# Kernel tuning notes

Measured on AMD Instinct MI355X. Metric: run time of the kernel, lower is better.

## Reference

```python
import jax, jax.numpy as jnp
import numpy as np
from jax import lax

E = 8          # num_experts
K = 2          # top-k
TASKS = 8
GATE_DIM = 16
# (in, expand, out, kernel, stride) per MoE stage
STAGES = [(3, 32, 16, 7, 2), (16, 64, 32, 3, 1), (32, 128, 64, 3, 2), (64, 256, 64, 3, 1), (64, 128, 32, 3, 1)]
DN = ('NCHW', 'OIHW', 'NCHW')


def _pw(x, w):
    return lax.conv_general_dilated(x, w, (1, 1), 'VALID', dimension_numbers=DN)


def _dw(x, w, s):
    p = w.shape[-1] // 2
    return lax.conv_general_dilated(x, w, (s, s), [(p, p), (p, p)], dimension_numbers=DN, feature_group_count=x.shape[1])


def _gn(x, scale, bias):
    # GroupNorm with num_groups = C // 4, eps = 1e-5 (torch default)
    B, C, H, W = x.shape
    G = C // 4
    xr = x.reshape(B, G, -1)
    m = xr.mean(-1, keepdims=True)
    v = xr.var(-1, keepdims=True)
    xn = ((xr - m) * lax.rsqrt(v + 1e-5)).reshape(B, C, H, W)
    return xn * scale[None, :, None, None] + bias[None, :, None, None]


def _dsc(x, p, stride):
    # DSCBlock: pw-conv -> GN -> SiLU -> dw-conv -> GN -> SiLU -> pw-conv -> GN
    w1, s1, b1, w2, s2, b2, w3, s3, b3 = p
    x = jax.nn.silu(_gn(_pw(x, w1), s1, b1))
    x = jax.nn.silu(_gn(_dw(x, w2, stride), s2, b2))
    return _gn(_pw(x, w3), s3, b3)


def _moe(gate_input, x, wg, p, stride, task_bh):
    # task-conditioned top-k softmax gating (noisy_gating=False, all aux loss weights 0)
    logits = gate_input @ wg[task_bh]                      # (B, E)
    probs = jax.nn.softmax(logits, axis=-1)
    topv, topi = lax.top_k(probs, K)
    topv = topv / topv.sum(-1, keepdims=True)              # renormalize top-k gates
    Bn = gate_input.shape[0]
    dense = jnp.zeros_like(probs).at[jnp.arange(Bn)[:, None], topi].set(topv)
    eo = jax.vmap(lambda pe: _dsc(x, pe, stride))(p)       # (E, B, C, H, W)
    return jnp.einsum('be,ebchw->bchw', dense, eo)


def _forward(fl, task_bh):
    gi, xi, ppe = fl[0], fl[1], fl[2]
    x = xi
    for i, (_, _, _, _, s) in enumerate(STAGES):
        base = 3 + i * 10
        wg = fl[base]
        p = tuple(fl[base + 1: base + 10])
        x = _moe(gi, x, wg, p, s, task_bh)
    Bn = x.shape[0]
    # patchify: (B,32,20,20) -> unfold(2,4,4).unfold(3,4,4) -> permute -> (B,25,512)
    patches = x.reshape(Bn, 32, 5, 4, 5, 4).transpose(0, 1, 2, 4, 3, 5)  # (B,32,5,5,4,4)
    patches = patches.transpose(0, 2, 3, 4, 5, 1).reshape(Bn, 25, 512)
    return patches + ppe


def setup_inputs():
    key = jax.random.key(0)
    ks = iter(jax.random.split(key, 256))
    B = 64
    d = {}
    d['gate_input'] = jax.random.normal(next(ks), (B, GATE_DIM), jnp.float32)
    d['expert_input'] = jax.random.normal(next(ks), (B, 3, 80, 80), jnp.float32)
    d['patch_pos_embed'] = 0.02 * jax.random.normal(next(ks), (1, 25, 512), jnp.float32)
    for i, (cin, exp, cout, k, s) in enumerate(STAGES, 1):
        d[f's{i}_wg'] = 0.1 * jax.random.normal(next(ks), (TASKS, GATE_DIM, E), jnp.float32)
        d[f's{i}_w1'] = jax.random.normal(next(ks), (E, exp, cin, 1, 1), jnp.float32) / np.sqrt(cin)
        d[f's{i}_g1s'] = 1.0 + 0.1 * jax.random.normal(next(ks), (E, exp), jnp.float32)
        d[f's{i}_g1b'] = 0.1 * jax.random.normal(next(ks), (E, exp), jnp.float32)
        d[f's{i}_w2'] = jax.random.normal(next(ks), (E, exp, 1, k, k), jnp.float32) / k
        d[f's{i}_g2s'] = 1.0 + 0.1 * jax.random.normal(next(ks), (E, exp), jnp.float32)
        d[f's{i}_g2b'] = 0.1 * jax.random.normal(next(ks), (E, exp), jnp.float32)
        d[f's{i}_w3'] = jax.random.normal(next(ks), (E, cout, exp, 1, 1), jnp.float32) / np.sqrt(exp)
        d[f's{i}_g3s'] = 1.0 + 0.1 * jax.random.normal(next(ks), (E, cout), jnp.float32)
        d[f's{i}_g3b'] = 0.1 * jax.random.normal(next(ks), (E, cout), jnp.float32)
    d['task_bh'] = 3
    return d


def reference(gate_input, expert_input, patch_pos_embed, s1_wg, s1_w1, s1_g1s, s1_g1b, s1_w2, s1_g2s, s1_g2b, s1_w3, s1_g3s, s1_g3b, s2_wg, s2_w1, s2_g1s, s2_g1b, s2_w2, s2_g2s, s2_g2b, s2_w3, s2_g3s, s2_g3b, s3_wg, s3_w1, s3_g1s, s3_g1b, s3_w2, s3_g2s, s3_g2b, s3_w3, s3_g3s, s3_g3b, s4_wg, s4_w1, s4_g1s, s4_g1b, s4_w2, s4_g2s, s4_g2b, s4_w3, s4_g3s, s4_g3b, s5_wg, s5_w1, s5_g1s, s5_g1b, s5_w2, s5_g2s, s5_g2b, s5_w3, s5_g3s, s5_g3b, task_bh):
    fl = (gate_input, expert_input, patch_pos_embed,
          s1_wg, s1_w1, s1_g1s, s1_g1b, s1_w2, s1_g2s, s1_g2b, s1_w3, s1_g3s, s1_g3b,
          s2_wg, s2_w1, s2_g1s, s2_g1b, s2_w2, s2_g2s, s2_g2b, s2_w3, s2_g3s, s2_g3b,
          s3_wg, s3_w1, s3_g1s, s3_g1b, s3_w2, s3_g2s, s3_g2b, s3_w3, s3_g3s, s3_g3b,
          s4_wg, s4_w1, s4_g1s, s4_g1b, s4_w2, s4_g2s, s4_g2b, s4_w3, s4_g3s, s4_g3b,
          s5_wg, s5_w1, s5_g1s, s5_g1b, s5_w2, s5_g2s, s5_g2b, s5_w3, s5_g3s, s5_g3b)
    patches = _forward(fl, task_bh)
    loss = jnp.zeros((), patches.dtype)  # all MoE loss weights are 0 in VisionEncoder
    return (patches, loss)
```

## Files before the change

### kernel.cpp

```cpp
#include <hip/hip_runtime.h>
#include <cstddef>

#define TPB 256

typedef __attribute__((ext_vector_type(8))) short short8v;
typedef __attribute__((ext_vector_type(4))) float f32x4;

__device__ __forceinline__ int rfl(int v) { return __builtin_amdgcn_readfirstlane(v); }
__device__ __forceinline__ float rflf(float v) {
    return __int_as_float(__builtin_amdgcn_readfirstlane(__float_as_int(v)));
}

__device__ __forceinline__ unsigned short f2bf(float f) {
    union { float f; unsigned int u; } x{f};
    unsigned int r = x.u + 0x7fffu + ((x.u >> 16) & 1u);
    return (unsigned short)(r >> 16);
}
__device__ __forceinline__ float bf2f(unsigned short u) {
    return __uint_as_float(((unsigned int)u) << 16);
}

template <int N, int NW>
__device__ __forceinline__ void bredN(float* v, float* red) {
    __syncthreads();
// ... 32 lines not shown
                                             unsigned short* __restrict__ whi) {
    const int sizes[9] = {4096, 8192, 16384, 32768, 65536, 131072, 131072, 65536, 32768};
    int idx = blockIdx.x * 256 + threadIdx.x;
    if (idx >= 487424) return;
    int rem = idx, s = 0;
    while (s < 8 && rem >= sizes[s]) { rem -= sizes[s]; s++; }
    whi[idx] = f2bf(wsrc.p[s][rem]);
}

__global__ void gate_kernel(const float* __restrict__ gi, GatePtrs gp,
                            const int* __restrict__ taskp,
                            int* __restrict__ gidx, float* __restrict__ gw) {
    const int s = blockIdx.x;
    const int b = threadIdx.x;
    const int task = taskp[0];
    const float* wg = gp.wg[s] + (size_t)task * 16 * 8;
    float l[8];
    #pragma unroll
    for (int e = 0; e < 8; e++) l[e] = 0.f;
    for (int d = 0; d < 16; d++) {
        float v = gi[b * 16 + d];
        #pragma unroll
        for (int e = 0; e < 8; e++) l[e] += v * wg[d * 8 + e];
    }
    float mx = l[0];
    #pragma unroll
    for (int e = 1; e < 8; e++) mx = fmaxf(mx, l[e]);
    float p[8]; float sum = 0.f;
    #pragma unroll
    for (int e = 0; e < 8; e++) { p[e] = expf(l[e] - mx); sum += p[e]; }
    int i0 = 0;
    #pragma unroll
    for (int e = 1; e < 8; e++) if (p[e] > p[i0]) i0 = e;
    int i1 = (i0 == 0) ? 1 : 0;
    #pragma unroll
    for (int e = 0; e < 8; e++) if (e != i0 && p[e] > p[i1]) i1 = e;
    const float denom = p[i0] + p[i1];
    const int base = (s * 64 + b) * 2;
    gidx[base] = i0; gidx[base + 1] = i1;
    gw[base] = p[i0] / denom; gw[base + 1] = p[i1] / denom;
}

template <int M, int K, int N, int MT, int NCHK, bool FOLD, bool BIN>
__global__ __launch_bounds__(256) void gemm_bf16(
    const unsigned short* __restrict__ inp,
    const unsigned short* __restrict__ whi,
    const int* __restrict__ gidx, const float* __restrict__ foldStats,
    const float* __restrict__ foldS, const float* __restrict__ foldB,
    unsigned short* __restrict__ outp, float* __restrict__ stats,
    int mfull, int moff, int nchk1) {
    constexpr int KITERS = (K + 31) / 32;
    constexpr int IM = (MT == 64) ? 2 : 1;
    constexpr int IN = (MT == 16) ? 1 : 2;
    const int bx = blockIdx.x;
    const int nc = bx % NCHK, mc = bx / NCHK;
    const int b = blockIdx.y, slot = blockIdx.z;
    const int bs = b * 2 + slot;
    const int e = rfl(gidx[b * 2 + slot]);
    const int n0 = nc * 64, m0 = mc * MT;
    const int tid = threadIdx.x;
    const int lane = tid & 63, wv = tid >> 6;
    const int quad = lane >> 4, l15 = lane & 15;

    __shared__ __align__(16) unsigned short wtile[MT * 40];
    __shared__ unsigned int intile[16 * 65];
    __shared__ float sred[(MT / 4) * 2];
    __shared__ float afv[K], bfv[K];

    if (tid < (MT / 4) * 2) sred[tid] = 0.f;
    if constexpr (FOLD) {
        for (int c = tid; c < K; c += 256) {
            const int g = c >> 2;
            float s1 = 0.f, s2 = 0.f;
            for (int i = 0; i < nchk1; i++) {
                s1 += foldStats[(((size_t)bs * (K / 4) + g) * nchk1 + i) * 2 + 0];
                s2 += foldStats[(((size_t)bs * (K / 4) + g) * nchk1 + i) * 2 + 1];
            }
            const float mean = s1 / (4.f * N);
            const float var = s2 / (4.f * N) - mean * mean;
            const float inv = rsqrtf(var + 1e-5f);
            const float sc = foldS[e * K + c], bi = foldB[e * K + c];
            afv[c] = inv * sc;
            bfv[c] = bi - mean * inv * sc;
        }
    }

    int mbase, nbase;
    if constexpr (MT == 64) { mbase = (wv & 1) * 32; nbase = (wv >> 1) * 32; }
    else if constexpr (MT == 32) { mbase = (wv & 1) * 16; nbase = (wv >> 1) * 32; }
    else { mbase = 0; nbase = wv * 16; }

    f32x4 acc[IM][IN];
    #pragma unroll
    for (int im = 0; im < IM; im++)
        #pragma unroll
        for (int in = 0; in < IN; in++)
            #pragma unroll
            for (int r = 0; r < 4; r++) acc[im][in][r] = 0.f;

    const unsigned short* ib = inp + (size_t)(BIN ? b : bs) * K * N;
    const unsigned short* wbH = whi + ((size_t)e * mfull + moff) * K;

    for (int k0 = 0; k0 < KITERS * 32; k0 += 32) {
        __syncthreads();
        for (int i = tid; i < MT * 32; i += 256) {
            const int m = i >> 5, kk = i & 31;
            const bool ok = (k0 + kk < K);
            wtile[m * 40 + kk] = ok ? wbH[(size_t)(m0 + m) * K + k0 + kk]
                                    : (unsigned short)0;
// ... 45 lines not shown
                    afr[im], bu.s, acc[im][in], 0, 0, 0);
        }
    }

    unsigned short* ob = outp + (size_t)bs * M * N;
    #pragma unroll
    for (int im = 0; im < IM; im++) {
        #pragma unroll
        for (int in = 0; in < IN; in++) {
            const int n = n0 + nbase + in * 16 + l15;
            float s1 = 0.f, s2 = 0.f;
            #pragma unroll
            for (int r = 0; r < 4; r++) {
                const float a = acc[im][in][r];
                s1 += a; s2 += a * a;
            }
            if (n < N) {
                #pragma unroll
                for (int r = 0; r < 4; r++) {
                    const int m = m0 + mbase + im * 16 + quad * 4 + r;
                    ob[(size_t)m * N + n] = f2bf(acc[im][in][r]);
                }
            }
            #pragma unroll
            for (int off = 8; off > 0; off >>= 1) {
                s1 += __shfl_down(s1, off, 16);
                s2 += __shfl_down(s2, off, 16);
            }
            if (l15 == 0) {
                const int gl = (mbase + im * 16) / 4 + quad;
                atomicAdd(&sred[gl * 2 + 0], s1);
                atomicAdd(&sred[gl * 2 + 1], s2);
            }
        }
    }
    __syncthreads();
    for (int i = tid; i < MT / 4; i += 256) {
        float* sp = stats + (((size_t)bs * (mfull / 4) + moff / 4 + mc * (MT / 4) + i)
                             * NCHK + nc) * 2;
        sp[0] = sred[i * 2]; sp[1] = sred[i * 2 + 1];
    }
}

template <int CLOC, int CFULL, int H, int W, int NCH, int TPBk, int NCHK1>
__global__ __launch_bounds__(TPBk) void dw_k(
    const unsigned short* __restrict__ raw1, const float* __restrict__ stats1,
    const float* __restrict__ g1s, const float* __restrict__ g1b,
    const float* __restrict__ w2, const int* __restrict__ gidx,
    unsigned short* __restrict__ act2raw, float* __restrict__ stats2, int coff) {
    constexpr int HW = H * W, HP = H + 2, WPL = W + 3;
    constexpr int NPV = HW / 4, NG = NCH / 4, NW = TPBk / 64;
    constexpr int Qc = HW / 4, QT = NCH * Qc, QI = (QT + TPBk - 1) / TPBk;
    constexpr int G1 = CFULL / 4;
    const int gch = blockIdx.x, b = blockIdx.y, slot = blockIdx.z;
    const int bs = b * 2 + slot;
    const int tid = threadIdx.x;
    const int e = rfl(gidx[b * 2 + slot]);
    const int cb0 = gch * NCH;
    const int cg0 = coff + cb0;

    __shared__ float buf1[NCH * HP * WPL];
    __shared__ float w2s[NCH * 9];
    __shared__ float afl[NCH], bfl[NCH];
    __shared__ float red[2 * NG * NW];

    for (int i = tid; i < NCH * HP * WPL; i += TPBk) buf1[i] = 0.f;
    if (tid < NCH * 9) w2s[tid] = w2[((size_t)e * CFULL + cg0) * 9 + tid];
    if (tid < NCH) {
        const int g = (cg0 + tid) >> 2;
        float s1 = 0.f, s2 = 0.f;
        for (int i = 0; i < NCHK1; i++) {
            s1 += stats1[(((size_t)bs * G1 + g) * NCHK1 + i) * 2 + 0];
            s2 += stats1[(((size_t)bs * G1 + g) * NCHK1 + i) * 2 + 1];
        }
        const float mean = s1 / (4.f * HW);
        const float var = s2 / (4.f * HW) - mean * mean;
        const float inv = rsqrtf(var + 1e-5f);
        const float sc = g1s[e * CFULL + cg0 + tid], bi = g1b[e * CFULL + cg0 + tid];
        afl[tid] = inv * sc; bfl[tid] = bi - mean * inv * sc;
    }
    __syncthreads();

    const unsigned short* rb = raw1 + (size_t)bs * CLOC * HW + (size_t)cb0 * HW;
    for (int i = tid; i < NCH * NPV; i += TPBk) {
        const int c = i / NPV, pv = i - c * NPV;
        const int p4 = pv * 4, ph = p4 / W, pwb = p4 - ph * W;
        const ushort4 u = *(const ushort4*)(rb + (size_t)c * HW + p4);
        const float a = afl[c], bb = bfl[c];
        float* bp = &buf1[(c * HP + ph + 1) * WPL + pwb + 1];
        bp[0] = silu_f(a * bf2f(u.x) + bb);
        bp[1] = silu_f(a * bf2f(u.y) + bb);
        bp[2] = silu_f(a * bf2f(u.z) + bb);
        bp[3] = silu_f(a * bf2f(u.w) + bb);
    }
    __syncthreads();

    float st2[2 * NG];
    #pragma unroll
    for (int i = 0; i < 2 * NG; i++) st2[i] = 0.f;
    unsigned short* ao = act2raw + (size_t)bs * CFULL * HW + (size_t)cg0 * HW;
    #pragma unroll
    for (int qi = 0; qi < QI; qi++) {
        const int q = tid + qi * TPBk;
        if (QI * TPBk == QT || q < QT) {
            const int c = q / Qc, qq = q - c * Qc;
            const int oh = qq % H, owb = (qq / H) * 4;
            float o[4] = {0.f, 0.f, 0.f, 0.f};
            #pragma unroll
            for (int kh = 0; kh < 3; kh++) {
                const int base = (c * HP + oh + kh) * WPL + owb;
                float r[6];
                #pragma unroll
                for (int i = 0; i < 6; i++) r[i] = buf1[base + i];
                const float wa = w2s[c * 9 + kh * 3 + 0];
                const float wb = w2s[c * 9 + kh * 3 + 1];
                const float wcc = w2s[c * 9 + kh * 3 + 2];
                #pragma unroll
                for (int t = 0; t < 4; t++)
                    o[t] += wa * r[t] + wb * r[t + 1] + wcc * r[t + 2];
            }
            ushort4 ov = {f2bf(o[0]), f2bf(o[1]), f2bf(o[2]), f2bf(o[3])};
            *(ushort4*)(ao + c * HW + oh * W + owb) = ov;
            #pragma unroll
            for (int t = 0; t < 4; t++) {
                if constexpr (NG == 1) { st2[0] += o[t]; st2[1] += o[t] * o[t]; }
                else {
                    const bool gs = (c >= 4);
                    float a0 = gs ? 0.f : o[t], a1 = gs ? o[t] : 0.f;
                    st2[0] += a0; st2[1] += a0 * a0;
                    st2[2] += a1; st2[3] += a1 * a1;
                }
            }
        }
    }
    bredN<2 * NG, NW>(st2, red);
    if (tid == 0) {
        #pragma unroll
        for (int g = 0; g < NG; g++) {
            stats2[((size_t)bs * G1 + cg0 / 4 + g) * 2 + 0] = st2[g * 2];
            stats2[((size_t)bs * G1 + cg0 / 4 + g) * 2 + 1] = st2[g * 2 + 1];
        }
    }
}

__global__ __launch_bounds__(256) void s1_stats(
    const float* __restrict__ xin, const float* __restrict__ w1,
    const int* __restrict__ gidx, float* __restrict__ stats1) {
    const int g = blockIdx.x, b = blockIdx.y, slot = blockIdx.z;
    const int tid = threadIdx.x;
    const int e = rfl(gidx[b * 2 + slot]);
    __shared__ float red[8];
    const float* xb = xin + (size_t)b * 3 * 6400;
    const float* w1e = w1 + ((size_t)e * 32 + g * 4) * 3;
    float wr[4][3];
    #pragma unroll
    for (int c = 0; c < 4; c++)
        #pragma unroll
        for (int k = 0; k < 3; k++) wr[c][k] = rflf(w1e[c * 3 + k]);
    float s[2] = {0.f, 0.f};
    #pragma unroll
    for (int j = 0; j < 7; j++) {
        const int i = j * 256 + tid;
        if (i < 1600) {
            const int p4 = i * 4;
            const float4 v0 = *(const float4*)(xb + p4);
            const float4 v1 = *(const float4*)(xb + 6400 + p4);
            const float4 v2 = *(const float4*)(xb + 12800 + p4);
            const float a0[4] = {v0.x, v0.y, v0.z, v0.w};
            const float a1[4] = {v1.x, v1.y, v1.z, v1.w};
            const float a2[4] = {v2.x, v2.y, v2.z, v2.w};
            #pragma unroll
            for (int t = 0; t < 4; t++)
                #pragma unroll
                for (int c = 0; c < 4; c++) {
                    float a = fmaf(wr[c][0], a0[t], fmaf(wr[c][1], a1[t], wr[c][2] * a2[t]));
                    s[0] += a; s[1] += a * a;
                }
        }
    }
    bredN<2, 4>(s, red);
    if (tid == 0) {
        float* sp = stats1 + ((size_t)(b * 2 + slot) * 8 + g) * 2;
        sp[0] = s[0]; sp[1] = s[1];
    }
}

__global__ __launch_bounds__(256) void s1_band(
    const float* __restrict__ xin, const float* __restrict__ w1,
    const float* __restrict__ g1s, const float* __restrict__ g1b,
    const float* __restrict__ w2, const int* __restrict__ gidx,
    const float* __restrict__ stats1,
    unsigned short* __restrict__ rawdw, float* __restrict__ stats2) {
    constexpr int NR = 25, RW = 91, EVO = 44;
    const int gb = blockIdx.x;
    const int g = gb >> 2, band = gb & 3;
    const int b = blockIdx.y, slot = blockIdx.z;
    const int tid = threadIdx.x;
    const int e = rfl(gidx[b * 2 + slot]);

    __shared__ float sbuf[4 * NR * RW];
    __shared__ float w2s[196];
    __shared__ float red[8];

    for (int i = tid; i < 4 * NR * RW; i += 256) sbuf[i] = 0.f;
    if (tid < 196) w2s[tid] = w2[((size_t)e * 32 + g * 4) * 49 + tid];

    const float* sp = stats1 + ((size_t)(b * 2 + slot) * 8 + g) * 2;
    const float s1v = rflf(sp[0]), s2v = rflf(sp[1]);
    const float mean = s1v / 25600.f;
    const float var = s2v / 25600.f - mean * mean;
    const float inv = rsqrtf(var + 1e-5f);

    const float* xb = xin + (size_t)b * 3 * 6400;
    const float* w1e = w1 + ((size_t)e * 32 + g * 4) * 3;
    float wr[4][3], sc1r[4], bi1r[4];
    #pragma unroll
    for (int c = 0; c < 4; c++) {
        #pragma unroll
        for (int k = 0; k < 3; k++) wr[c][k] = rflf(w1e[c * 3 + k]);
        sc1r[c] = rflf(g1s[e * 32 + g * 4 + c]);
        bi1r[c] = rflf(g1b[e * 32 + g * 4 + c]);
    }
    const int oh0 = band * 10;
    const int rlo = 2 * oh0 - 3;
    __syncthreads();

    for (int ii = tid; ii < 500; ii += 256) {
        const int p4 = ii * 4;
        const int l = p4 / 80, pw = p4 - l * 80;
        const int r = rlo + l;
        if (r >= 0 && r < 80) {
            const int lrow = (l >> 1) + (l & 1) * 13;
            const float4 v0 = *(const float4*)(xb + r * 80 + pw);
            const float4 v1 = *(const float4*)(xb + 6400 + r * 80 + pw);
            const float4 v2 = *(const float4*)(xb + 12800 + r * 80 + pw);
            const float a0[4] = {v0.x, v0.y, v0.z, v0.w};
            const float a1[4] = {v1.x, v1.y, v1.z, v1.w};
            const float a2[4] = {v2.x, v2.y, v2.z, v2.w};
            #pragma unroll
            for (int c = 0; c < 4; c++) {
                #pragma unroll
                for (int t = 0; t < 4; t++) {
                    float a = fmaf(wr[c][0], a0[t], fmaf(wr[c][1], a1[t], wr[c][2] * a2[t]));
                    float v = silu_f((a - mean) * inv * sc1r[c] + bi1r[c]);
                    const int cc = pw + t + 3;
                    const int sl = (cc & 1) ? EVO + (cc >> 1) : (cc >> 1);
                    sbuf[(c * NR + lrow) * RW + sl] = v;
                }
            }
// ... 2 lines not shown
    __syncthreads();

    float st2[2] = {0.f, 0.f};
    unsigned short* rw = rawdw + (size_t)(b * 2 + slot) * 32 * 1600
                         + (size_t)g * 4 * 1600;
    #pragma unroll
    for (int qi = 0; qi < 2; qi++) {
        const int q = tid + qi * 256;
        if (q < 400) {
            const int c = q / 100;
            const int rem = q - c * 100;
            const int ohl = rem % 10, owb = (rem / 10) * 4;
            float o[4] = {0.f, 0.f, 0.f, 0.f};
            #pragma unroll
            for (int kh = 0; kh < 7; kh++) {
                const int lrow = ohl + (kh >> 1) + (kh & 1) * 13;
                const int base = (c * NR + lrow) * RW;
                const float2 e01 = *(const float2*)&sbuf[base + owb];
                const float2 e23 = *(const float2*)&sbuf[base + owb + 2];
                const float2 e45 = *(const float2*)&sbuf[base + owb + 4];
                const float e6 = sbuf[base + owb + 6];
                const float2 q01 = *(const float2*)&sbuf[base + EVO + owb];
                const float2 q23 = *(const float2*)&sbuf[base + EVO + owb + 2];
                const float2 q45 = *(const float2*)&sbuf[base + EVO + owb + 4];
                const float evr[7] = {e01.x, e01.y, e23.x, e23.y, e45.x, e45.y, e6};
                const float odr[6] = {q01.x, q01.y, q23.x, q23.y, q45.x, q45.y};
                const float w0 = w2s[c * 49 + kh * 7 + 0];
                const float w1v = w2s[c * 49 + kh * 7 + 1];
                const float w2v = w2s[c * 49 + kh * 7 + 2];
                const float w3 = w2s[c * 49 + kh * 7 + 3];
                const float w4 = w2s[c * 49 + kh * 7 + 4];
                const float w5 = w2s[c * 49 + kh * 7 + 5];
                const float w6 = w2s[c * 49 + kh * 7 + 6];
                #pragma unroll
                for (int t = 0; t < 4; t++)
                    o[t] += w0 * evr[t] + w1v * odr[t] + w2v * evr[t + 1]
                          + w3 * odr[t + 1] + w4 * evr[t + 2] + w5 * odr[t + 2]
                          + w6 * evr[t + 3];
            }
            const int oh = oh0 + ohl;
            ushort4 ov = {f2bf(o[0]), f2bf(o[1]), f2bf(o[2]), f2bf(o[3])};
            *(ushort4*)(rw + c * 1600 + oh * 40 + owb) = ov;
            #pragma unroll
            for (int t = 0; t < 4; t++) { st2[0] += o[t]; st2[1] += o[t] * o[t]; }
        }
    }
    bredN<2, 4>(st2, red);
    if (tid == 0) {
        float* s2p = stats2 + (((size_t)(b * 2 + slot) * 8 + g) * 4 + band) * 2;
        s2p[0] = st2[0]; s2p[1] = st2[1];
    }
}

template <int CIN, int CEXP, int KS, int STRIDE, int H, int W, int HO, int WO,
          int NCH, int TPBk>
__global__ __launch_bounds__(TPBk) void dsc_ab_v2(
    const unsigned short* __restrict__ xin, const float* __restrict__ w1,
    const float* __restrict__ g1s, const float* __restrict__ g1b,
    const float* __restrict__ w2,
    const float* __restrict__ g2s, const float* __restrict__ g2b,
    const int* __restrict__ gidx, unsigned short* __restrict__ act2) {
    constexpr int HW = H * W, HWO = HO * WO;
    constexpr int HP = H + 2, WPL = W + 3, EVW = (W + 2) / 2;
    constexpr int NPV = HW / 4;
    constexpr int JN = (NPV + TPBk - 1) / TPBk;
    constexpr int NW = TPBk / 64;
    constexpr int NG = NCH / 4;
    constexpr int Qc = HWO / 4;
    constexpr int QT = NCH * Qc;
    constexpr int QI = (QT + TPBk - 1) / TPBk;
    constexpr int KK = KS * KS;
    const int gch = blockIdx.x, b = blockIdx.y, slot = blockIdx.z;
    const int tid = threadIdx.x;
    const int e = rfl(gidx[b * 2 + slot]);
    const int cb0 = gch * NCH;

    __shared__ float buf1[NCH * HP * WPL];
    __shared__ float w2s[NCH * KK];
    __shared__ float sc2s[NCH], bi2s[NCH];
    __shared__ float red[2 * NG * NW];

    for (int i = tid; i < NCH * HP * WPL; i += TPBk) buf1[i] = 0.f;
    for (int i = tid; i < NCH * KK; i += TPBk) {
        int c = i / KK, k = i - c * KK;
        w2s[i] = w2[((size_t)e * CEXP + cb0 + c) * KK + k];
    }
    if (tid < NCH) {
        sc2s[tid] = g2s[e * CEXP + cb0 + tid];
        bi2s[tid] = g2b[e * CEXP + cb0 + tid];
    }

    const unsigned short* xb = xin + (size_t)b * CIN * HW;
    const float* w1e = w1 + ((size_t)e * CEXP + cb0) * CIN;

    float acc[NCH][JN][4];
    #pragma unroll
    for (int c = 0; c < NCH; c++)
        #pragma unroll
        for (int j = 0; j < JN; j++)
            #pragma unroll
            for (int t = 0; t < 4; t++) acc[c][j][t] = 0.f;

    for (int cb = 0; cb < CIN; cb += 4) {
        float wr[NCH][4];
        #pragma unroll
        for (int c = 0; c < NCH; c++)
            #pragma unroll
            for (int k = 0; k < 4; k++) wr[c][k] = rflf(w1e[c * CIN + cb + k]);
        #pragma unroll
        for (int j = 0; j < JN; j++) {
            const int pv = tid + j * TPBk;
            if (JN * TPBk == NPV || pv < NPV) {
                #pragma unroll
                for (int k = 0; k < 4; k++) {
                    const ushort4 v4 = *(const ushort4*)(xb + (cb + k) * HW + pv * 4);
                    const float va[4] = {bf2f(v4.x), bf2f(v4.y), bf2f(v4.z), bf2f(v4.w)};
                    #pragma unroll
                    for (int c = 0; c < NCH; c++)
                        #pragma unroll
                        for (int t = 0; t < 4; t++)
                            acc[c][j][t] = fmaf(wr[c][k], va[t], acc[c][j][t]);
                }
            }
        }
    }
    float st[2 * NG];
    #pragma unroll
    for (int i = 0; i < 2 * NG; i++) st[i] = 0.f;
    #pragma unroll
    for (int c = 0; c < NCH; c++) {
        const int gs = (c >> 2) * 2;
        #pragma unroll
        for (int j = 0; j < JN; j++)
            #pragma unroll
            for (int t = 0; t < 4; t++) {
                float a = acc[c][j][t];
                st[gs] += a; st[gs + 1] += a * a;
            }
    }
    bredN<2 * NG, NW>(st, red);
    float mg[NG], ig[NG];
    #pragma unroll
    for (int g = 0; g < NG; g++) {
        mg[g] = st[g * 2] / (4.f * HW);
        float var = st[g * 2 + 1] / (4.f * HW) - mg[g] * mg[g];
        ig[g] = rsqrtf(var + 1e-5f);
    }
    float sc1r[NCH], bi1r[NCH];
    #pragma unroll
    for (int c = 0; c < NCH; c++) {
        sc1r[c] = rflf(g1s[e * CEXP + cb0 + c]);
        bi1r[c] = rflf(g1b[e * CEXP + cb0 + c]);
    }
    #pragma unroll
    for (int j = 0; j < JN; j++) {
        const int pv = tid + j * TPBk;
        if (JN * TPBk == NPV || pv < NPV) {
            const int p4 = pv * 4;
            const int ph = p4 / W, pwb = p4 - ph * W;
            #pragma unroll
            for (int c = 0; c < NCH; c++) {
                const int g = (NG == 1) ? 0 : (c >> 2);
                #pragma unroll
                for (int t = 0; t < 4; t++) {
                    float v = silu_f((acc[c][j][t] - mg[g]) * ig[g] * sc1r[c] + bi1r[c]);
                    const int j2 = pwb + t + 1;
                    const int col = (STRIDE == 1) ? j2
                                    : ((j2 & 1) ? EVW + (j2 >> 1) : (j2 >> 1));
                    buf1[(c * HP + ph + 1) * WPL + col] = v;
                }
            }
        }
    }
    __syncthreads();

    float dacc[QI][4];
    float st2[2 * NG];
    #pragma unroll
    for (int i = 0; i < 2 * NG; i++) st2[i] = 0.f;
    #pragma unroll
    for (int qi = 0; qi < QI; qi++) {
        #pragma unroll
        for (int t = 0; t < 4; t++) dacc[qi][t] = 0.f;
        const int q = tid + qi * TPBk;
        if (QI * TPBk == QT || q < QT) {
            const int c = q / Qc, qq = q - c * Qc;
            const int oh = qq % HO, owb = (qq / HO) * 4;
            float o[4] = {0.f, 0.f, 0.f, 0.f};
            if (STRIDE == 1) {
                #pragma unroll
                for (int kh = 0; kh < KS; kh++) {
                    const int base = (c * HP + oh + kh) * WPL + owb;
                    float r[6];
                    #pragma unroll
                    for (int i = 0; i < 6; i++) r[i] = buf1[base + i];
                    const float wa = w2s[c * KK + kh * KS + 0];
                    const float wb = w2s[c * KK + kh * KS + 1];
                    const float wcc = w2s[c * KK + kh * KS + 2];
                    #pragma unroll
                    for (int t = 0; t < 4; t++)
                        o[t] += wa * r[t] + wb * r[t + 1] + wcc * r[t + 2];
                }
            } else {
                #pragma unroll
                for (int kh = 0; kh < KS; kh++) {
                    const int base = (c * HP + 2 * oh + kh) * WPL;
                    float ev[5], od[4];
                    #pragma unroll
                    for (int i = 0; i < 5; i++) ev[i] = buf1[base + owb + i];
                    #pragma unroll
                    for (int i = 0; i < 4; i++) od[i] = buf1[base + EVW + owb + i];
                    const float wa = w2s[c * KK + kh * KS + 0];
                    const float wb = w2s[c * KK + kh * KS + 1];
                    const float wcc = w2s[c * KK + kh * KS + 2];
                    #pragma unroll
                    for (int t = 0; t < 4; t++)
                        o[t] += wa * ev[t] + wb * od[t] + wcc * ev[t + 1];
                }
            }
            #pragma unroll
            for (int t = 0; t < 4; t++) {
                float a = o[t];
                dacc[qi][t] = a;
                if constexpr (NG == 1) {
                    st2[0] += a; st2[1] += a * a;
                } else {
                    const bool gsel = (c >= 4);
                    float a0 = gsel ? 0.f : a, a1 = gsel ? a : 0.f;
                    st2[0] += a0; st2[1] += a0 * a0;
                    st2[2] += a1; st2[3] += a1 * a1;
                }
            }
        }
    }
    bredN<2 * NG, NW>(st2, red);
    float m2[NG], i2[NG];
    #pragma unroll
    for (int g = 0; g < NG; g++) {
        m2[g] = st2[g * 2] / (4.f * HWO);
        float var = st2[g * 2 + 1] / (4.f * HWO) - m2[g] * m2[g];
        i2[g] = rsqrtf(var + 1e-5f);
    }
    unsigned short* ao = act2 + ((size_t)(b * 2 + slot) * CEXP + cb0) * HWO;
    #pragma unroll
    for (int qi = 0; qi < QI; qi++) {
        const int q = tid + qi * TPBk;
        if (QI * TPBk == QT || q < QT) {
            const int c = q / Qc, qq = q - c * Qc;
            const int oh = qq % HO, owb = (qq / HO) * 4;
            const int g = (NG == 1) ? 0 : ((c >= 4) ? 1 : 0);
            const float sc = sc2s[c], bi = bi2s[c];
            ushort4 ov;
            ov.x = f2bf(silu_f((dacc[qi][0] - m2[g]) * i2[g] * sc + bi));
            ov.y = f2bf(silu_f((dacc[qi][1] - m2[g]) * i2[g] * sc + bi));
            ov.z = f2bf(silu_f((dacc[qi][2] - m2[g]) * i2[g] * sc + bi));
            ov.w = f2bf(silu_f((dacc[qi][3] - m2[g]) * i2[g] * sc + bi));
            *(ushort4*)(ao + c * HWO + oh * WO + owb) = ov;
        }
    }
}

template <int COUT, int HWO, int PXC, bool PATCH>
__global__ __launch_bounds__(256) void pw3_k3m(
    const unsigned short* __restrict__ raw3, const float* __restrict__ statsw,
    const float* __restrict__ g3s, const float* __restrict__ g3b,
    const int* __restrict__ gidx, const float* __restrict__ gw,
    const float* __restrict__ ppe, float* __restrict__ outf,
    unsigned short* __restrict__ outb) {
    constexpr int G = COUT / 4;
    constexpr int Q = HWO / 4;
    const int gg = blockIdx.x, b = blockIdx.y;
    const int tid = threadIdx.x;

    float A[2][4], Bv[2][4];
    #pragma unroll
    for (int slot = 0; slot < 2; slot++) {
        const int e = rfl(gidx[b * 2 + slot]);
        const float wgt = rflf(gw[b * 2 + slot]);
        const float* sp = statsw + ((size_t)(b * 2 + slot) * G + gg) * PXC * 2;
        float s1 = 0.f, s2 = 0.f;
        for (int i = 0; i < PXC; i++) { s1 += rflf(sp[i * 2]); s2 += rflf(sp[i * 2 + 1]); }
        const float mean = s1 / (4.f * HWO);
        const float var = s2 / (4.f * HWO) - mean * mean;
        const float inv = rsqrtf(var + 1e-5f);
        #pragma unroll
        for (int i = 0; i < 4; i++) {
            const int c = gg * 4 + i;
            const float sc = rflf(g3s[e * COUT + c]);
            const float bi = rflf(g3b[e * COUT + c]);
            A[slot][i] = wgt * inv * sc;
            Bv[slot][i] = wgt * (bi - mean * inv * sc);
        }
    }

    #pragma unroll
    for (int i = 0; i < 4; i++) {
        const int c = gg * 4 + i;
        const unsigned short* r0 = raw3 + ((size_t)(b * 2 + 0) * COUT + c) * HWO;
        const unsigned short* r1 = raw3 + ((size_t)(b * 2 + 1) * COUT + c) * HWO;
        for (int q = tid; q < Q; q += 256) {
            const int p4 = q * 4;
            const ushort4 u0 = *(const ushort4*)(r0 + p4);
            const ushort4 u1 = *(const ushort4*)(r1 + p4);
            const float v0[4] = {bf2f(u0.x), bf2f(u0.y), bf2f(u0.z), bf2f(u0.w)};
            const float v1[4] = {bf2f(u1.x), bf2f(u1.y), bf2f(u1.z), bf2f(u1.w)};
            float o[4];
            #pragma unroll
            for (int t = 0; t < 4; t++)
                o[t] = fmaf(A[0][i], v0[t], Bv[0][i]) + fmaf(A[1][i], v1[t], Bv[1][i]);
            if constexpr (!PATCH) {
                ushort4 ov = {f2bf(o[0]), f2bf(o[1]), f2bf(o[2]), f2bf(o[3])};
                *(ushort4*)(outb + ((size_t)b * COUT + c) * HWO + p4) = ov;
            } else {
                const int ph = p4 / 20, pw0 = p4 - ph * 20;
                const int p = (ph >> 2) * 5 + (pw0 >> 2);
                const int dbase = ((ph & 3) * 4) * 32 + c;
                float* op = outf + ((size_t)b * 25 + p) * 512;
                const float* pp = ppe + p * 512;
                #pragma unroll
                for (int jj = 0; jj < 4; jj++)
                    op[dbase + jj * 32] = o[jj] + pp[dbase + jj * 32];
            }
        }
    }
    if (PATCH && gg == 0 && b == 0 && tid == 0) outf[64 * 25 * 512] = 0.f;
}

extern "C" void kernel_launch(void* const* d_in, const int* in_sizes, int n_in,
                              void* d_out, int out_size, void* d_ws, size_t ws_size,
                              hipStream_t stream) {
    const float* gate_input = (const float*)d_in[0];
    const float* expert_input = (const float*)d_in[1];
    const float* ppe = (const float*)d_in[2];
    const int* taskp = (const int*)d_in[53];
    auto in = [&](int s, int k) { return (const float*)d_in[3 + s * 10 + k]; };

    char* ws = (char*)d_ws;
    int* gidx = (int*)ws;
    float* gw = (float*)(ws + 4096);
    size_t off = 8192;
    unsigned short* x0 = (unsigned short*)(ws + off); off += (size_t)8 << 20;
    unsigned short* x1 = (unsigned short*)(ws + off); off += (size_t)8 << 20;
    unsigned short* act2 = (unsigned short*)(ws + off); off += (size_t)27 << 20;
    char* bufA = ws + off; off += (size_t)27 << 20;
    float* stats1 = (float*)(ws + off); off += (size_t)2 << 20;
    float* stats2 = (float*)(ws + off); off += 262144;
    float* stats3 = (float*)(ws + off); off += (size_t)1 << 20;
    float* st1a = (float*)(ws + off); off += 65536;
    float* st1b = (float*)(ws + off); off += 65536;
    unsigned short* whi = (unsigned short*)(ws + off); off += 487424 * 2;
    float* outp = (float*)d_out;
    unsigned short* bufA16 = (unsigned short*)bufA;

    WSrcs wsrc;
    wsrc.p[0] = in(0, 7); wsrc.p[1] = in(1, 1); wsrc.p[2] = in(1, 7);
    wsrc.p[3] = in(2, 1); wsrc.p[4] = in(2, 7); wsrc.p[5] = in(3, 1);
    wsrc.p[6] = in(3, 7); wsrc.p[7] = in(4, 1); wsrc.p[8] = in(4, 7);

    GatePtrs gp;
    for (int s = 0; s < 5; s++) gp.wg[s] = in(s, 0);
    gate_kernel<<<5, 64, 0, stream>>>(gate_input, gp, taskp, gidx, gw);
    wprep<<<(487424 + 255) / 256, 256, 0, stream>>>(wsrc, whi);

    s1_stats<<<dim3(8, 64, 2), 256, 0, stream>>>(expert_input, in(0, 1),
                                                 gidx + 0 * 128, st1a);
    s1_band<<<dim3(32, 64, 2), 256, 0, stream>>>(
        expert_input, in(0, 1), in(0, 2), in(0, 3), in(0, 4),
        gidx + 0 * 128, st1a, bufA16, st1b);
    gemm_bf16<16, 32, 1600, 16, 25, true, false><<<dim3(25, 64, 2), 256, 0, stream>>>(
        bufA16, whi + 0, gidx + 0 * 128, st1b, in(0, 5), in(0, 6),
        act2, stats3, 16, 0, 4);
    pw3_k3m<16, 1600, 25, false><<<dim3(4, 64), 256, 0, stream>>>(
        act2, stats3, in(0, 8), in(0, 9), gidx + 0 * 128,
        gw + 0 * 128, ppe, nullptr, x0);

    gemm_bf16<64, 16, 1600, 64, 25, false, true><<<dim3(25, 64, 2), 256, 0, stream>>>(
        x0, whi + 4096, gidx + 1 * 128, nullptr, nullptr, nullptr,
        bufA16, stats1, 64, 0, 1);
    dw_k<64, 64, 40, 40, 4, 256, 25><<<dim3(16, 64, 2), 256, 0, stream>>>(
        bufA16, stats1, in(1, 2), in(1, 3), in(1, 4),
        gidx + 1 * 128, act2, stats2, 0);
    gemm_bf16<32, 64, 1600, 32, 25, true, false><<<dim3(25, 64, 2), 256, 0, stream>>>(
        act2, whi + 12288, gidx + 1 * 128, stats2, in(1, 5), in(1, 6),
        bufA16, stats3, 32, 0, 1);
    pw3_k3m<32, 1600, 25, false><<<dim3(8, 64), 256, 0, stream>>>(
        bufA16, stats3, in(1, 8), in(1, 9), gidx + 1 * 128,
        gw + 1 * 128, ppe, nullptr, x1);

    dsc_ab_v2<32, 128, 3, 2, 40, 40, 20, 20, 4, 256><<<dim3(32, 64, 2), 256, 0, stream>>>(
        x1, in(2, 1), in(2, 2), in(2, 3), in(2, 4), in(2, 5), in(2, 6),
        gidx + 2 * 128, act2);
    gemm_bf16<64, 128, 400, 64, 7, false, false><<<dim3(7, 64, 2), 256, 0, stream>>>(
        act2, whi + 61440, gidx + 2 * 128, nullptr, nullptr, nullptr,
        bufA16, stats3, 64, 0, 1);
    pw3_k3m<64, 400, 7, false><<<dim3(16, 64), 256, 0, stream>>>(
        bufA16, stats3, in(2, 8), in(2, 9), gidx + 2 * 128,
        gw + 2 * 128, ppe, nullptr, x0);

    gemm_bf16<256, 64, 400, 64, 7, false, true><<<dim3(28, 64, 2), 256, 0, stream>>>(
        x0, whi + 126976, gidx + 3 * 128, nullptr, nullptr, nullptr,
        bufA16, stats1, 256, 0, 1);
    dw_k<256, 256, 20, 20, 8, 128, 7><<<dim3(32, 64, 2), 128, 0, stream>>>(
        bufA16, stats1, in(3, 2), in(3, 3), in(3, 4),
        gidx + 3 * 128, act2, stats2, 0);
    gemm_bf16<64, 256, 400, 64, 7, true, false><<<dim3(7, 64, 2), 256, 0, stream>>>(
        act2, whi + 258048, gidx + 3 * 128, stats2, in(3, 5), in(3, 6),
        bufA16, stats3, 64, 0, 1);
    pw3_k3m<64, 400, 7, false><<<dim3(16, 64), 256, 0, stream>>>(
        bufA16, stats3, in(3, 8), in(3, 9), gidx + 3 * 128,
        gw + 3 * 128, ppe, nullptr, x1);

    gemm_bf16<128, 64, 400, 64, 7, false, true><<<dim3(14, 64, 2), 256, 0, stream>>>(
        x1, whi + 389120, gidx + 4 * 128, nullptr, nullptr, nullptr,
        bufA16, stats1, 128, 0, 1);
    dw_k<128, 128, 20, 20, 8, 128, 7><<<dim3(16, 64, 2), 128, 0, stream>>>(
        bufA16, stats1, in(4, 2), in(4, 3), in(4, 4),
        gidx + 4 * 128, act2, stats2, 0);
    gemm_bf16<32, 128, 400, 32, 7, true, false><<<dim3(7, 64, 2), 256, 0, stream>>>(
        act2, whi + 454656, gidx + 4 * 128, stats2, in(4, 5), in(4, 6),
        bufA16, stats3, 32, 0, 1);
    pw3_k3m<32, 400, 7, true><<<dim3(8, 64), 256, 0, stream>>>(
        bufA16, stats3, in(4, 8), in(4, 9), gidx + 4 * 128,
        gw + 4 * 128, ppe, outp, nullptr);
}
```

Measured before the change: 495.2 us.

## Swap grid order to batch-major and share stage-3 input loads across both top-k slots

```diff
diff --git a/kernel.cpp b/kernel.cpp
--- a/kernel.cpp
+++ b/kernel.cpp
@@ -108,9 +108,10 @@
     constexpr int KITERS = (K + 31) / 32;
     constexpr int IM = (MT == 64) ? 2 : 1;
     constexpr int IN = (MT == 16) ? 1 : 2;
-    const int bx = blockIdx.x;
+    const int b = blockIdx.x;
+    const int bx = blockIdx.y;
     const int nc = bx % NCHK, mc = bx / NCHK;
-    const int b = blockIdx.y, slot = blockIdx.z;
+    const int slot = blockIdx.z;
     const int bs = b * 2 + slot;
     const int e = rfl(gidx[b * 2 + slot]);
     const int n0 = nc * 64, m0 = mc * MT;
@@ -262,7 +263,7 @@
     constexpr int NPV = HW / 4, NG = NCH / 4, NW = TPBk / 64;
     constexpr int Qc = HW / 4, QT = NCH * Qc, QI = (QT + TPBk - 1) / TPBk;
     constexpr int G1 = CFULL / 4;
-    const int gch = blockIdx.x, b = blockIdx.y, slot = blockIdx.z;
+    const int b = blockIdx.x, gch = blockIdx.y, slot = blockIdx.z;
     const int bs = b * 2 + slot;
     const int tid = threadIdx.x;
     const int e = rfl(gidx[b * 2 + slot]);
@@ -356,7 +357,7 @@
 __global__ __launch_bounds__(256) void s1_stats(
     const float* __restrict__ xin, const float* __restrict__ w1,
     const int* __restrict__ gidx, float* __restrict__ stats1) {
-    const int g = blockIdx.x, b = blockIdx.y, slot = blockIdx.z;
+    const int b = blockIdx.x, g = blockIdx.y, slot = blockIdx.z;
     const int tid = threadIdx.x;
     const int e = rfl(gidx[b * 2 + slot]);
     __shared__ float red[8];
@@ -402,9 +403,10 @@
     const float* __restrict__ stats1,
     unsigned short* __restrict__ rawdw, float* __restrict__ stats2) {
     constexpr int NR = 25, RW = 91, EVO = 44;
-    const int gb = blockIdx.x;
+    const int b = blockIdx.x;
+    const int gb = blockIdx.y;
     const int g = gb >> 2, band = gb & 3;
-    const int b = blockIdx.y, slot = blockIdx.z;
+    const int slot = blockIdx.z;
     const int tid = threadIdx.x;
     const int e = rfl(gidx[b * 2 + slot]);
 
@@ -513,210 +515,184 @@
     }
 }
 
-template <int CIN, int CEXP, int KS, int STRIDE, int H, int W, int HO, int WO,
-          int NCH, int TPBk>
-__global__ __launch_bounds__(TPBk) void dsc_ab_v2(
+__global__ __launch_bounds__(256) void dsc_ab_s3(
     const unsigned short* __restrict__ xin, const float* __restrict__ w1,
     const float* __restrict__ g1s, const float* __restrict__ g1b,
     const float* __restrict__ w2,
     const float* __restrict__ g2s, const float* __restrict__ g2b,
     const int* __restrict__ gidx, unsigned short* __restrict__ act2) {
-    constexpr int HW = H * W, HWO = HO * WO;
+    constexpr int CIN = 32, CEXP = 128, H = 40, W = 40, HW = 1600;
+    constexpr int HO = 20, WO = 20, HWO = 400;
     constexpr int HP = H + 2, WPL = W + 3, EVW = (W + 2) / 2;
-    constexpr int NPV = HW / 4;
-    constexpr int JN = (NPV + TPBk - 1) / TPBk;
-    constexpr int NW = TPBk / 64;
-    constexpr int NG = NCH / 4;
-    constexpr int Qc = HWO / 4;
-    constexpr int QT = NCH * Qc;
-    constexpr int QI = (QT + TPBk - 1) / TPBk;
-    constexpr int KK = KS * KS;
-    const int gch = blockIdx.x, b = blockIdx.y, slot = blockIdx.z;
+    const int b = blockIdx.x, gch = blockIdx.y;
+    const int cb0 = gch * 4;
     const int tid = threadIdx.x;
-    const int e = rfl(gidx[b * 2 + slot]);
-    const int cb0 = gch * NCH;
-
-    __shared__ float buf1[NCH * HP * WPL];
-    __shared__ float w2s[NCH * KK];
-    __shared__ float sc2s[NCH], bi2s[NCH];
-    __shared__ float red[2 * NG * NW];
-
-    for (int i = tid; i < NCH * HP * WPL; i += TPBk) buf1[i] = 0.f;
-    for (int i = tid; i < NCH * KK; i += TPBk) {
-        int c = i / KK, k = i - c * KK;
-        w2s[i] = w2[((size_t)e * CEXP + cb0 + c) * KK + k];
-    }
-    if (tid < NCH) {
-        sc2s[tid] = g2s[e * CEXP + cb0 + tid];
-        bi2s[tid] = g2b[e * CEXP + cb0 + tid];
+    int ee[2];
+    ee[0] = rfl(gidx[b * 2 + 0]);
+    ee[1] = rfl(gidx[b * 2 + 1]);
+
+    __shared__ float buf1[4 * HP * WPL];
+    __shared__ float w2s[2][36];
+    __shared__ float sc2s[2][4], bi2s[2][4];
+    __shared__ float red[16];
+
+    for (int i = tid; i < 4 * HP * WPL; i += 256) buf1[i] = 0.f;
+    if (tid < 72) {
+        const int s = tid / 36, i = tid - s * 36;
+        w2s[s][i] = w2[((size_t)ee[s] * CEXP + cb0) * 9 + i];
+    }
+    if (tid < 8) {
+        const int s = tid >> 2, c = tid & 3;
+        sc2s[s][c] = g2s[ee[s] * CEXP + cb0 + c];
+        bi2s[s][c] = g2b[ee[s] * CEXP + cb0 + c];
     }
 
     const unsigned short* xb = xin + (size_t)b * CIN * HW;
-    const float* w1e = w1 + ((size_t)e * CEXP + cb0) * CIN;
-
-    float acc[NCH][JN][4];
-    #pragma unroll
-    for (int c = 0; c < NCH; c++)
-        #pragma unroll
-        for (int j = 0; j < JN; j++)
-            #pragma unroll
-            for (int t = 0; t < 4; t++) acc[c][j][t] = 0.f;
+
+    float acc[2][4][2][4];
+    #pragma unroll
+    for (int s = 0; s < 2; s++)
+        #pragma unroll
+        for (int c = 0; c < 4; c++)
+            #pragma unroll
+            for (int j = 0; j < 2; j++)
+                #pragma unroll
+                for (int t = 0; t < 4; t++) acc[s][c][j][t] = 0.f;
 
     for (int cb = 0; cb < CIN; cb += 4) {
-        float wr[NCH][4];
-        #pragma unroll
-        for (int c = 0; c < NCH; c++)
-            #pragma unroll
-            for (int k = 0; k < 4; k++) wr[c][k] = rflf(w1e[c * CIN + cb + k]);
-        #pragma unroll
-        for (int j = 0; j < JN; j++) {
-            const int pv = tid + j * TPBk;
-            if (JN * TPBk == NPV || pv < NPV) {
+        float wr[2][4][4];
+        #pragma unroll
+        for (int s = 0; s < 2; s++) {
+            const float* w1e = w1 + ((size_t)ee[s] * CEXP + cb0) * CIN;
+            #pragma unroll
+            for (int c = 0; c < 4; c++)
+                #pragma unroll
+                for (int k = 0; k < 4; k++)
+                    wr[s][c][k] = rflf(w1e[c * CIN + cb + k]);
+        }
+        #pragma unroll
+        for (int j = 0; j < 2; j++) {
+            const int pv = tid + j * 256;
+            if (pv < 400) {
                 #pragma unroll
                 for (int k = 0; k < 4; k++) {
                     const ushort4 v4 = *(const ushort4*)(xb + (cb + k) * HW + pv * 4);
                     const float va[4] = {bf2f(v4.x), bf2f(v4.y), bf2f(v4.z), bf2f(v4.w)};
                     #pragma unroll
-                    for (int c = 0; c < NCH; c++)
+                    for (int s = 0; s < 2; s++)
                         #pragma unroll
-                        for (int t = 0; t < 4; t++)
-                            acc[c][j][t] = fmaf(wr[c][k], va[t], acc[c][j][t]);
-                }
-            }
-        }
-    }
-    float st[2 * NG];
-    #pragma unroll
-    for (int i = 0; i < 2 * NG; i++) st[i] = 0.f;
-    #pragma unroll
-    for (int c = 0; c < NCH; c++) {
-        const int gs = (c >> 2) * 2;
-        #pragma unroll
-        for (int j = 0; j < JN; j++)
-            #pragma unroll
-            for (int t = 0; t < 4; t++) {
-                float a = acc[c][j][t];
-                st[gs] += a; st[gs + 1] += a * a;
-            }
-    }
-    bredN<2 * NG, NW>(st, red);
-    float mg[NG], ig[NG];
-    #pragma unroll
-    for (int g = 0; g < NG; g++) {
-        mg[g] = st[g * 2] / (4.f * HW);
-        float var = st[g * 2 + 1] / (4.f * HW) - mg[g] * mg[g];
-        ig[g] = rsqrtf(var + 1e-5f);
-    }
-    float sc1r[NCH], bi1r[NCH];
-    #pragma unroll
-    for (int c = 0; c < NCH; c++) {
-        sc1r[c] = rflf(g1s[e * CEXP + cb0 + c]);
-        bi1r[c] = rflf(g1b[e * CEXP + cb0 + c]);
-    }
-    #pragma unroll
-    for (int j = 0; j < JN; j++) {
-        const int pv = tid + j * TPBk;
-        if (JN * TPBk == NPV || pv < NPV) {
-            const int p4 = pv * 4;
-            const int ph = p4 / W, pwb = p4 - ph * W;
-            #pragma unroll
-            for (int c = 0; c < NCH; c++) {
-                const int g = (NG == 1) ? 0 : (c >> 2);
+                        for (int c = 0; c < 4; c++)
+                            #pragma unroll
+                            for (int t = 0; t < 4; t++)
+                                acc[s][c][j][t] = fmaf(wr[s][c][k], va[t], acc[s][c][j][t]);
+                }
+            }
+        }
+    }
+    float st[4] = {0.f, 0.f, 0.f, 0.f};
+    #pragma unroll
+    for (int s = 0; s < 2; s++)
+        #pragma unroll
+        for (int c = 0; c < 4; c++)
+            #pragma unroll
+            for (int j = 0; j < 2; j++)
                 #pragma unroll
                 for (int t = 0; t < 4; t++) {
-                    float v = silu_f((acc[c][j][t] - mg[g]) * ig[g] * sc1r[c] + bi1r[c]);
-                    const int j2 = pwb + t + 1;
-                    const int col = (STRIDE == 1) ? j2
-                                    : ((j2 & 1) ? EVW + (j2 >> 1) : (j2 >> 1));
-                    buf1[(c * HP + ph + 1) * WPL + col] = v;
-                }
-            }
-        }
-    }
-    __syncthreads();
-
-    float dacc[QI][4];
-    float st2[2 * NG];
-    #pragma unroll
-    for (int i = 0; i < 2 * NG; i++) st2[i] = 0.f;
-    #pragma unroll
-    for (int qi = 0; qi < QI; qi++) {
-        #pragma unroll
-        for (int t = 0; t < 4; t++) dacc[qi][t] = 0.f;
-        const int q = tid + qi * TPBk;
-        if (QI * TPBk == QT || q < QT) {
-            const int c = q / Qc, qq = q - c * Qc;
-            const int oh = qq % HO, owb = (qq / HO) * 4;
-            float o[4] = {0.f, 0.f, 0.f, 0.f};
-            if (STRIDE == 1) {
-                #pragma unroll
-                for (int kh = 0; kh < KS; kh++) {
-                    const int base = (c * HP + oh + kh) * WPL + owb;
-                    float r[6];
+                    const float a = acc[s][c][j][t];
+                    st[s * 2] += a; st[s * 2 + 1] += a * a;
+                }
+    bredN<4, 4>(st, red);
+    float mg[2], ig[2], sc1r[2][4], bi1r[2][4];
+    #pragma unroll
+    for (int s = 0; s < 2; s++) {
+        mg[s] = st[s * 2] / 6400.f;
+        const float var = st[s * 2 + 1] / 6400.f - mg[s] * mg[s];
+        ig[s] = rsqrtf(var + 1e-5f);
+        #pragma unroll
+        for (int c = 0; c < 4; c++) {
+            sc1r[s][c] = rflf(g1s[ee[s] * CEXP + cb0 + c]);
+            bi1r[s][c] = rflf(g1b[ee[s] * CEXP + cb0 + c]);
+        }
+    }
+
+    float dacc[2][2][4];
+    float st2[4] = {0.f, 0.f, 0.f, 0.f};
+    #pragma unroll
+    for (int s = 0; s < 2; s++) {
+        if (s) __syncthreads();
+        #pragma unroll
+        for (int j = 0; j < 2; j++) {
+            const int pv = tid + j * 256;
+            if (pv < 400) {
+                const int p4 = pv * 4;
+                const int ph = p4 / W, pwb = p4 - ph * W;
+                #pragma unroll
+                for (int c = 0; c < 4; c++) {
                     #pragma unroll
-                    for (int i = 0; i < 6; i++) r[i] = buf1[base + i];
-                    const float wa = w2s[c * KK + kh * KS + 0];
-                    const float wb = w2s[c * KK + kh * KS + 1];
-                    const float wcc = w2s[c * KK + kh * KS + 2];
-                    #pragma unroll
-                    for (int t = 0; t < 4; t++)
-                        o[t] += wa * r[t] + wb * r[t + 1] + wcc * r[t + 2];
-                }
-            } else {
-                #pragma unroll
-                for (int kh = 0; kh < KS; kh++) {
+                    for (int t = 0; t < 4; t++) {
+                        const float v = silu_f((acc[s][c][j][t] - mg[s]) * ig[s]
+                                               * sc1r[s][c] + bi1r[s][c]);
+                        const int j2 = pwb + t + 1;
+                        const int col = (j2 & 1) ? EVW + (j2 >> 1) : (j2 >> 1);
+                        buf1[(c * HP + ph + 1) * WPL + col] = v;
+                    }
+                }
+            }
+        }
+        __syncthreads();
+        #pragma unroll
+        for (int qi = 0; qi < 2; qi++) {
+            #pragma unroll
+            for (int t = 0; t < 4; t++) dacc[s][qi][t] = 0.f;
+            const int q = tid + qi * 256;
+            if (q < 400) {
+                const int c = q / 100, qq = q - c * 100;
+                const int oh = qq % HO, owb = (qq / HO) * 4;
+                float o[4] = {0.f, 0.f, 0.f, 0.f};
+                #pragma unroll
+                for (int kh = 0; kh < 3; kh++) {
                     const int base = (c * HP + 2 * oh + kh) * WPL;
                     float ev[5], od[4];
                     #pragma unroll
                     for (int i = 0; i < 5; i++) ev[i] = buf1[base + owb + i];
                     #pragma unroll
                     for (int i = 0; i < 4; i++) od[i] = buf1[base + EVW + owb + i];
-                    const float wa = w2s[c * KK + kh * KS + 0];
-                    const float wb = w2s[c * KK + kh * KS + 1];
-                    const float wcc = w2s[c * KK + kh * KS + 2];
+                    const float wa = w2s[s][c * 9 + kh * 3 + 0];
+                    const float wb = w2s[s][c * 9 + kh * 3 + 1];
+                    const float wcc = w2s[s][c * 9 + kh * 3 + 2];
                     #pragma unroll
                     for (int t = 0; t < 4; t++)
                         o[t] += wa * ev[t] + wb * od[t] + wcc * ev[t + 1];
                 }
-            }
-            #pragma unroll
-            for (int t = 0; t < 4; t++) {
-                float a = o[t];
-                dacc[qi][t] = a;
-                if constexpr (NG == 1) {
-                    st2[0] += a; st2[1] += a * a;
-                } else {
-                    const bool gsel = (c >= 4);
-                    float a0 = gsel ? 0.f : a, a1 = gsel ? a : 0.f;
-                    st2[0] += a0; st2[1] += a0 * a0;
-                    st2[2] += a1; st2[3] += a1 * a1;
-                }
-            }
-        }
-    }
-    bredN<2 * NG, NW>(st2, red);
-    float m2[NG], i2[NG];
-    #pragma unroll
-    for (int g = 0; g < NG; g++) {
-        m2[g] = st2[g * 2] / (4.f * HWO);
-        float var = st2[g * 2 + 1] / (4.f * HWO) - m2[g] * m2[g];
-        i2[g] = rsqrtf(var + 1e-5f);
-    }
-    unsigned short* ao = act2 + ((size_t)(b * 2 + slot) * CEXP + cb0) * HWO;
-    #pragma unroll
-    for (int qi = 0; qi < QI; qi++) {
-        const int q = tid + qi * TPBk;
-        if (QI * TPBk == QT || q < QT) {
-            const int c = q / Qc, qq = q - c * Qc;
-            const int oh = qq % HO, owb = (qq / HO) * 4;
-            const int g = (NG == 1) ? 0 : ((c >= 4) ? 1 : 0);
-            const float sc = sc2s[c], bi = bi2s[c];
-            ushort4 ov;
-            ov.x = f2bf(silu_f((dacc[qi][0] - m2[g]) * i2[g] * sc + bi));
-            ov.y = f2bf(silu_f((dacc[qi][1] - m2[g]) * i2[g] * sc + bi));
-            ov.z = f2bf(silu_f((dacc[qi][2] - m2[g]) * i2[g] * sc + bi));
-            ov.w = f2bf(silu_f((dacc[qi][3] - m2[g]) * i2[g] * sc + bi));
-            *(ushort4*)(ao + c * HWO + oh * WO + owb) = ov;
+                #pragma unroll
+                for (int t = 0; t < 4; t++) {
+                    dacc[s][qi][t] = o[t];
+                    st2[s * 2] += o[t]; st2[s * 2 + 1] += o[t] * o[t];
+                }
+            }
+        }
+    }
+    bredN<4, 4>(st2, red);
+    #pragma unroll
+    for (int s = 0; s < 2; s++) {
+        const float m2 = st2[s * 2] / 1600.f;
+        const float var2 = st2[s * 2 + 1] / 1600.f - m2 * m2;
+        const float i2 = rsqrtf(var2 + 1e-5f);
+        unsigned short* ao = act2 + ((size_t)(b * 2 + s) * CEXP + cb0) * HWO;
+        #pragma unroll
+        for (int qi = 0; qi < 2; qi++) {
+            const int q = tid + qi * 256;
+            if (q < 400) {
+                const int c = q / 100, qq = q - c * 100;
+                const int oh = qq % HO, owb = (qq / HO) * 4;
+                const float sc = sc2s[s][c], bi = bi2s[s][c];
+                ushort4 ov;
+                ov.x = f2bf(silu_f((dacc[s][qi][0] - m2) * i2 * sc + bi));
+                ov.y = f2bf(silu_f((dacc[s][qi][1] - m2) * i2 * sc + bi));
+                ov.z = f2bf(silu_f((dacc[s][qi][2] - m2) * i2 * sc + bi));
+                ov.w = f2bf(silu_f((dacc[s][qi][3] - m2) * i2 * sc + bi));
+                *(ushort4*)(ao + c * HWO + oh * WO + owb) = ov;
+            }
         }
     }
 }
@@ -730,7 +706,7 @@
     unsigned short* __restrict__ outb) {
     constexpr int G = COUT / 4;
     constexpr int Q = HWO / 4;
-    const int gg = blockIdx.x, b = blockIdx.y;
+    const int b = blockIdx.x, gg = blockIdx.y;
     const int tid = threadIdx.x;
 
     float A[2][4], Bv[2][4];
@@ -823,64 +799,64 @@
     gate_kernel<<<5, 64, 0, stream>>>(gate_input, gp, taskp, gidx, gw);
     wprep<<<(487424 + 255) / 256, 256, 0, stream>>>(wsrc, whi);
 
-    s1_stats<<<dim3(8, 64, 2), 256, 0, stream>>>(expert_input, in(0, 1),
+    s1_stats<<<dim3(64, 8, 2), 256, 0, stream>>>(expert_input, in(0, 1),
                                                  gidx + 0 * 128, st1a);
-    s1_band<<<dim3(32, 64, 2), 256, 0, stream>>>(
+    s1_band<<<dim3(64, 32, 2), 256, 0, stream>>>(
         expert_input, in(0, 1), in(0, 2), in(0, 3), in(0, 4),
         gidx + 0 * 128, st1a, bufA16, st1b);
-    gemm_bf16<16, 32, 1600, 16, 25, true, false><<<dim3(25, 64, 2), 256, 0, stream>>>(
+    gemm_bf16<16, 32, 1600, 16, 25, true, false><<<dim3(64, 25, 2), 256, 0, stream>>>(
         bufA16, whi + 0, gidx + 0 * 128, st1b, in(0, 5), in(0, 6),
         act2, stats3, 16, 0, 4);
-    pw3_k3m<16, 1600, 25, false><<<dim3(4, 64), 256, 0, stream>>>(
+    pw3_k3m<16, 1600, 25, false><<<dim3(64, 4), 256, 0, stream>>>(
         act2, stats3, in(0, 8), in(0, 9), gidx + 0 * 128,
         gw + 0 * 128, ppe, nullptr, x0);
 
-    gemm_bf16<64, 16, 1600, 64, 25, false, true><<<dim3(25, 64, 2), 256, 0, stream>>>(
+    gemm_bf16<64, 16, 1600, 64, 25, false, true><<<dim3(64, 25, 2), 256, 0, stream>>>(
         x0, whi + 4096, gidx + 1 * 128, nullptr, nullptr, nullptr,
         bufA16, stats1, 64, 0, 1);
-    dw_k<64, 64, 40, 40, 4, 256, 25><<<dim3(16, 64, 2), 256, 0, stream>>>(
+    dw_k<64, 64, 40, 40, 4, 256, 25><<<dim3(64, 16, 2), 256, 0, stream>>>(
         bufA16, stats1, in(1, 2), in(1, 3), in(1, 4),
         gidx + 1 * 128, act2, stats2, 0);
-    gemm_bf16<32, 64, 1600, 32, 25, true, false><<<dim3(25, 64, 2), 256, 0, stream>>>(
+    gemm_bf16<32, 64, 1600, 32, 25, true, false><<<dim3(64, 25, 2), 256, 0, stream>>>(
         act2, whi + 12288, gidx + 1 * 128, stats2, in(1, 5), in(1, 6),
         bufA16, stats3, 32, 0, 1);
-    pw3_k3m<32, 1600, 25, false><<<dim3(8, 64), 256, 0, stream>>>(
+    pw3_k3m<32, 1600, 25, false><<<dim3(64, 8), 256, 0, stream>>>(
         bufA16, stats3, in(1, 8), in(1, 9), gidx + 1 * 128,
         gw + 1 * 128, ppe, nullptr, x1);
 
-    dsc_ab_v2<32, 128, 3, 2, 40, 40, 20, 20, 4, 256><<<dim3(32, 64, 2), 256, 0, stream>>>(
+    dsc_ab_s3<<<dim3(64, 32), 256, 0, stream>>>(
         x1, in(2, 1), in(2, 2), in(2, 3), in(2, 4), in(2, 5), in(2, 6),
         gidx + 2 * 128, act2);
-    gemm_bf16<64, 128, 400, 64, 7, false, false><<<dim3(7, 64, 2), 256, 0, stream>>>(
+    gemm_bf16<64, 128, 400, 64, 7, false, false><<<dim3(64, 7, 2), 256, 0, stream>>>(
         act2, whi + 61440, gidx + 2 * 128, nullptr, nullptr, nullptr,
         bufA16, stats3, 64, 0, 1);
-    pw3_k3m<64, 400, 7, false><<<dim3(16, 64), 256, 0, stream>>>(
+    pw3_k3m<64, 400, 7, false><<<dim3(64, 16), 256, 0, stream>>>(
         bufA16, stats3, in(2, 8), in(2, 9), gidx + 2 * 128,
         gw + 2 * 128, ppe, nullptr, x0);
 
-    gemm_bf16<256, 64, 400, 64, 7, false, true><<<dim3(28, 64, 2), 256, 0, stream>>>(
+    gemm_bf16<256, 64, 400, 64, 7, false, true><<<dim3(64, 28, 2), 256, 0, stream>>>(
         x0, whi + 126976, gidx + 3 * 128, nullptr, nullptr, nullptr,
         bufA16, stats1, 256, 0, 1);
-    dw_k<256, 256, 20, 20, 8, 128, 7><<<dim3(32, 64, 2), 128, 0, stream>>>(
+    dw_k<256, 256, 20, 20, 8, 128, 7><<<dim3(64, 32, 2), 128, 0, stream>>>(
         bufA16, stats1, in(3, 2), in(3, 3), in(3, 4),
         gidx + 3 * 128, act2, stats2, 0);
-    gemm_bf16<64, 256, 400, 64, 7, true, false><<<dim3(7, 64, 2), 256, 0, stream>>>(
+    gemm_bf16<64, 256, 400, 64, 7, true, false><<<dim3(64, 7, 2), 256, 0, stream>>>(
         act2, whi + 258048, gidx + 3 * 128, stats2, in(3, 5), in(3, 6),
         bufA16, stats3, 64, 0, 1);
-    pw3_k3m<64, 400, 7, false><<<dim3(16, 64), 256, 0, stream>>>(
+    pw3_k3m<64, 400, 7, false><<<dim3(64, 16), 256, 0, stream>>>(
         bufA16, stats3, in(3, 8), in(3, 9), gidx + 3 * 128,
         gw + 3 * 128, ppe, nullptr, x1);
 
-    gemm_bf16<128, 64, 400, 64, 7, false, true><<<dim3(14, 64, 2), 256, 0, stream>>>(
+    gemm_bf16<128, 64, 400, 64, 7, false, true><<<dim3(64, 14, 2), 256, 0, stream>>>(
         x1, whi + 389120, gidx + 4 * 128, nullptr, nullptr, nullptr,
         bufA16, stats1, 128, 0, 1);
-    dw_k<128, 128, 20, 20, 8, 128, 7><<<dim3(16, 64, 2), 128, 0, stream>>>(
+    dw_k<128, 128, 20, 20, 8, 128, 7><<<dim3(64, 16, 2), 128, 0, stream>>>(
         bufA16, stats1, in(4, 2), in(4, 3), in(4, 4),
         gidx + 4 * 128, act2, stats2, 0);
-    gemm_bf16<32, 128, 400, 32, 7, true, false><<<dim3(7, 64, 2), 256, 0, stream>>>(
+    gemm_bf16<32, 128, 400, 32, 7, true, false><<<dim3(64, 7, 2), 256, 0, stream>>>(
         act2, whi + 454656, gidx + 4 * 128, stats2, in(4, 5), in(4, 6),
         bufA16, stats3, 32, 0, 1);
-    pw3_k3m<32, 400, 7, true><<<dim3(8, 64), 256, 0, stream>>>(
+    pw3_k3m<32, 400, 7, true><<<dim3(64, 8), 256, 0, stream>>>(
         bufA16, stats3, in(4, 8), in(4, 9), gidx + 4 * 128,
         gw + 4 * 128, ppe, outp, nullptr);
 }
```

After: 555.1 us. 12.1% more time.
